# Kernel optimization log

Measured on AMD Instinct MI355X. Metric: run time of the kernel, lower is better.

Reference implementation:

```python
import jax, jax.numpy as jnp
import numpy as np
import math
from jax import lax

B, NP1, M, D, H, L, DFF = 16, 65, 256, 512, 8, 3, 2048
EPS_PROJ = 0.01  # MartingaleProjectionLayer is built with epsilon=0.01
LN_EPS = 1e-5


def _pos_encoding(n, d):
    pos = np.arange(n, dtype=np.float32)[:, None]
    div = np.exp(np.arange(0, d, 2, dtype=np.float32) * (-math.log(10000.0) / d))
    pe = np.zeros((n, d), dtype=np.float32)
    pe[:, 0::2] = np.sin(pos * div)
    pe[:, 1::2] = np.cos(pos * div)
    return jnp.asarray(pe)


def setup_inputs() -> dict:
    key = jax.random.key(0)
    ks = jax.random.split(key, 32)
    s = 0.02
    marg = jax.random.uniform(ks[0], (B, NP1, M), jnp.float32)
    marg = marg / marg.sum(axis=-1, keepdims=True)  # proper distributions
    return {
        "marginals": marg,
        "x_grid": jnp.linspace(-3.0, 3.0, M, dtype=jnp.float32),
        "conv_w": jax.random.normal(ks[1], (128, 1, 5), jnp.float32) * s,
        "conv_b": jax.random.normal(ks[2], (128,), jnp.float32) * s,
        "fc_w": jax.random.normal(ks[3], (128, D), jnp.float32) * s,
        "fc_b": jax.random.normal(ks[4], (D,), jnp.float32) * s,
        "ln0_g": jnp.ones((D,), jnp.float32),
        "ln0_b": jnp.zeros((D,), jnp.float32),
        "pos_enc": _pos_encoding(NP1, D),
        "qkv_w": jax.random.normal(ks[5], (L, 3 * D, D), jnp.float32) * s,
        "qkv_b": jax.random.normal(ks[6], (L, 3 * D), jnp.float32) * s,
        "out_w": jax.random.normal(ks[7], (L, D, D), jnp.float32) * s,
        "out_b": jax.random.normal(ks[8], (L, D), jnp.float32) * s,
        "ln1_g": jnp.ones((L, D), jnp.float32),
        "ln1_b": jnp.zeros((L, D), jnp.float32),
        "ff1_w": jax.random.normal(ks[9], (L, DFF, D), jnp.float32) * s,
        "ff1_b": jax.random.normal(ks[10], (L, DFF), jnp.float32) * s,
        "ff2_w": jax.random.normal(ks[11], (L, D, DFF), jnp.float32) * s,
        "ff2_b": jax.random.normal(ks[12], (L, D), jnp.float32) * s,
        "ln2_g": jnp.ones((L, D), jnp.float32),
        "ln2_b": jnp.zeros((L, D), jnp.float32),
        "u_w": jax.random.normal(ks[13], (M, D), jnp.float32) * s,
        "u_b": jax.random.normal(ks[14], (M,), jnp.float32) * s,
        "h_w": jax.random.normal(ks[15], (M, D), jnp.float32) * s,
        "h_b": jax.random.normal(ks[16], (M,), jnp.float32) * s,
    }


def _ln(x, g, b):
    mu = x.mean(axis=-1, keepdims=True)
    var = ((x - mu) ** 2).mean(axis=-1, keepdims=True)
    return (x - mu) * lax.rsqrt(var + LN_EPS) * g + b


def _gelu(x):
    return jax.nn.gelu(x, approximate=False)  # torch default exact GELU


def reference(marginals, x_grid, conv_w, conv_b, fc_w, fc_b, ln0_g, ln0_b,
              pos_enc, qkv_w, qkv_b, out_w, out_b, ln1_g, ln1_b,
              ff1_w, ff1_b, ff2_w, ff2_b, ln2_g, ln2_b, u_w, u_b, h_w, h_b):
    b, np1, m = marginals.shape
    n = np1 - 1
    d = fc_w.shape[1]
    nh = H
    dh = d // nh

    # ---- marginal embedding: Conv1d(1,128,k=5,pad=2) -> mean over grid -> FC+LN+GELU
    x = marginals.reshape(b * np1, 1, m)
    y = lax.conv_general_dilated(x, conv_w, (1,), [(2, 2)],
                                 dimension_numbers=("NCH", "OIH", "NCH"))
    y = y + conv_b[None, :, None]          # (b*np1, 128, m)
    emb = y.mean(axis=2)                   # (b*np1, 128)
    emb = _gelu(_ln(emb @ fc_w + fc_b, ln0_g, ln0_b))
    xs = emb.reshape(b, np1, d) + pos_enc[None, :np1, :]

    # ---- post-norm transformer encoder (dropout off / eval mode)
    scale = 1.0 / math.sqrt(dh)
    for l in range(L):
        qkv = xs @ qkv_w[l].T + qkv_b[l]                        # (b, s, 3d)
        q, k, v = jnp.split(qkv, 3, axis=-1)
        q = q.reshape(b, np1, nh, dh).transpose(0, 2, 1, 3)
        k = k.reshape(b, np1, nh, dh).transpose(0, 2, 1, 3)
        v = v.reshape(b, np1, nh, dh).transpose(0, 2, 1, 3)
        att = jax.nn.softmax(jnp.einsum("bhqd,bhkd->bhqk", q, k) * scale, axis=-1)
        o = jnp.einsum("bhqk,bhkd->bhqd", att, v)
        o = o.transpose(0, 2, 1, 3).reshape(b, np1, d)
        o = o @ out_w[l].T + out_b[l]
        xs = _ln(xs + o, ln1_g[l], ln1_b[l])
        ff = _gelu(xs @ ff1_w[l].T + ff1_b[l]) @ ff2_w[l].T + ff2_b[l]
        xs = _ln(xs + ff, ln2_g[l], ln2_b[l])

    u_pot = xs @ u_w.T + u_b                                    # (b, np1, M)
    h_raw = xs[:, :n, :] @ h_w.T + h_b                          # (b, n, M)

    # ---- vectorized martingale projection over all N timesteps
    x_diff = x_grid[:, None] - x_grid[None, :]                  # (M, M)
    h_kernel = h_raw[..., None] * x_diff                        # (b, n, M, M)
    P = jax.nn.softmax(h_kernel / EPS_PROJ, axis=-1)
    expected_next = jnp.einsum("bnij,j->bni", P, x_grid)
    drift = expected_next - x_grid                              # (b, n, M)
    mu = marginals[:, :n, :]
    weight_drift = (mu * drift).sum(axis=-1, keepdims=True)
    correction = weight_drift / (mu.sum(axis=-1, keepdims=True) + 1e-8)
    h_pot = h_raw - correction
    return (u_pot, h_pot)
```

## Files before the change

kernel.cpp:

```cpp
#include <hip/hip_runtime.h>
#include <math.h>


#define BT   1040
#define NP1  65
#define Dm   512
#define MG   256

typedef short short8 __attribute__((ext_vector_type(8)));
typedef float f32x4  __attribute__((ext_vector_type(4)));
typedef unsigned short u16;

__device__ __forceinline__ size_t pidx(int r, int c, int KB) {
  return ((size_t)((r >> 6) * KB + (c >> 6)) * 8 + ((c & 63) >> 3)) * 512
       + (size_t)((r & 63) * 8 + (c & 7));
}

__device__ __forceinline__ u16 f2bf(float f) {
  unsigned int u = __float_as_uint(f);
  u += 0x7FFF + ((u >> 16) & 1);
  return (u16)(u >> 16);
}

__device__ __forceinline__ float bf2f(u16 v) {
  return __uint_as_float((unsigned int)v << 16);
}

__device__ __forceinline__ float gelu_exact(float x) {
  return 0.5f * x * (1.0f + erff(x * 0.70710678118654752f));
}

__device__ __forceinline__ void async16(const u16* g, u16* l) {
  __builtin_amdgcn_global_load_lds(
      (const __attribute__((address_space(1))) unsigned int*)g,
      (__attribute__((address_space(3))) unsigned int*)l, 16, 0, 0);
}

__device__ __forceinline__ float wred(float v) {
#pragma unroll
  for (int o = 32; o; o >>= 1) v += __shfl_xor(v, o, 64);
  return v;
}

__device__ __forceinline__ float block_reduce_sum(float v, float* s) {
#pragma unroll
  for (int off = 32; off; off >>= 1) v += __shfl_down(v, off, 64);
  int lane = threadIdx.x & 63, wid = threadIdx.x >> 6;
  __syncthreads();
  if (lane == 0) s[wid] = v;
  __syncthreads();
  return s[0] + s[1] + s[2] + s[3];
}

__device__ __forceinline__ float f_closed(float a) {
  const float tf = 2.3529411765f;
  float t = a * tf;
  float s = fabsf(t);
  float E;
  if (s < 1e-4f) {
    E = 127.5f - 5461.25f * t;
  } else {
    float u = s * 256.0f;
    float term2 = (u < 80.0f) ? 256.0f / expm1f(u) : 0.0f;
    float Epos = 1.0f / expm1f(s) - term2;
    E = (t > 0.0f) ? Epos : 255.0f - Epos;
  }
  return -3.0f + 0.0235294118f * E;
}

__global__ __launch_bounds__(256) void prep_kernel(
    const float* __restrict__ qkv_w, const float* __restrict__ out_w,
    const float* __restrict__ ff1_w, const float* __restrict__ ff2_w,
    const float* __restrict__ u_w,   const float* __restrict__ h_w,
    u16* __restrict__ wdst,
    const float* __restrict__ marg, const float* __restrict__ conv_w,
    const float* __restrict__ conv_b, const float* __restrict__ fc_w,
    const float* __restrict__ fc_b, const float* __restrict__ g,
    const float* __restrict__ bb, const float* __restrict__ pos,
    float* __restrict__ xs, u16* __restrict__ xsb)
{
  const int tid = threadIdx.x;
  if (blockIdx.x < 512) {
    const size_t O1 = 2359296, O2 = 3145728, O3 = 6291456;
    const size_t O4 = 9437184, O5 = 9568256, TOT4 = 9699328 / 4;
    for (size_t e4 = (size_t)blockIdx.x * 256 + tid; e4 < TOT4;
         e4 += (size_t)512 * 256) {
      size_t e = e4 * 4;
      const float* src; size_t base; int n, k, KB;
      if (e < O1)      { size_t r = e;      src = qkv_w + r; base = 0;
                         n = (int)(r >> 9);  k = (int)(r & 511);  KB = 8; }
      else if (e < O2) { size_t r = e - O1; src = out_w + r; base = O1;
                         n = (int)(r >> 9);  k = (int)(r & 511);  KB = 8; }
      else if (e < O3) { size_t r = e - O2; src = ff1_w + r; base = O2;
                         n = (int)(r >> 9);  k = (int)(r & 511);  KB = 8; }
      else if (e < O4) { size_t r = e - O3; src = ff2_w + r; base = O3;
                         n = (int)(r >> 11); k = (int)(r & 2047); KB = 32; }
      else if (e < O5) { size_t r = e - O4; src = u_w + r;   base = O4;
                         n = (int)(r >> 9);  k = (int)(r & 511);  KB = 8; }
      else             { size_t r = e - O5; src = h_w + r;   base = O4;
                         n = 256 + (int)(r >> 9); k = (int)(r & 511); KB = 8; }
      float4 v = *(const float4*)src;
      unsigned int lo = (unsigned int)f2bf(v.x) | ((unsigned int)f2bf(v.y) << 16);
      unsigned int hi = (unsigned int)f2bf(v.z) | ((unsigned int)f2bf(v.w) << 16);
      *(uint2*)(wdst + base + pidx(n, k, KB)) = make_uint2(lo, hi);
    }
    return;
  }
  __shared__ float es[4][128];
  __shared__ float sS[4];
  __shared__ float edge[4][4];
  __shared__ float red[4];
  const int t0 = (blockIdx.x - 512) * 4;
  const int lane = tid & 63, wave = tid >> 6;
  {
    float4 mv = *(const float4*)(marg + (size_t)(t0 + wave) * MG + lane * 4);
    float S = wred(mv.x + mv.y + mv.z + mv.w);
    if (lane == 0) sS[wave] = S;
  }
  if (tid < 16) {
    int k = tid >> 2, e = tid & 3;
    int idx = (e < 2) ? e : (e + 252);
    edge[k][e] = marg[(size_t)(t0 + k) * MG + idx];
  }
  __syncthreads();
  if (tid < 128) {
    int o = tid;
    float w0 = conv_w[o*5+0], w1 = conv_w[o*5+1], w2 = conv_w[o*5+2];
    float w3 = conv_w[o*5+3], w4 = conv_w[o*5+4], cb = conv_b[o];
#pragma unroll
    for (int k = 0; k < 4; ++k) {
      float S = sS[k];
      float x0 = edge[k][0], x1 = edge[k][1], x254 = edge[k][2], x255 = edge[k][3];
      es[k][o] = (w0*(S - x254 - x255) + w1*(S - x255) + w2*S
                + w3*(S - x0) + w4*(S - x0 - x1)) * (1.0f/256.0f) + cb;
    }
  }
  __syncthreads();
  float b0 = fc_b[tid], b1 = fc_b[tid + 256];
  float z[4][2];
#pragma unroll
  for (int k = 0; k < 4; ++k) { z[k][0] = b0; z[k][1] = b1; }
#pragma unroll 4
  for (int o = 0; o < 128; ++o) {
    float f0 = fc_w[(size_t)o*Dm + tid];
    float f1 = fc_w[(size_t)o*Dm + tid + 256];
#pragma unroll
    for (int k = 0; k < 4; ++k) {
      float e = es[k][o];
      z[k][0] += e * f0; z[k][1] += e * f1;
    }
  }
  float g0 = g[tid], g1 = g[tid+256], e0 = bb[tid], e1 = bb[tid+256];
#pragma unroll
  for (int k = 0; k < 4; ++k) {
    float mu = block_reduce_sum(z[k][0] + z[k][1], red) * (1.0f/512.0f);
    float d0 = z[k][0] - mu, d1 = z[k][1] - mu;
    float var = block_reduce_sum(d0*d0 + d1*d1, red) * (1.0f/512.0f);
    float inv = rsqrtf(var + 1e-5f);
    int t = t0 + k, p = t % NP1;
    float y0 = gelu_exact(d0*inv*g0 + e0) + pos[(size_t)p*Dm + tid];
    float y1 = gelu_exact(d1*inv*g1 + e1) + pos[(size_t)p*Dm + tid + 256];
    xs[(size_t)t*Dm + tid]        = y0;
    xs[(size_t)t*Dm + tid + 256]  = y1;
    xsb[pidx(t, tid, 8)]          = f2bf(y0);
    xsb[pidx(t, tid + 256, 8)]    = f2bf(y1);
  }
}

template<int MODE>
__global__ __launch_bounds__(256) void gemm_mfma(
    const u16* __restrict__ A, const u16* __restrict__ Bw,
    const float* __restrict__ bias, float* __restrict__ Cf,
    u16* __restrict__ Cb, int Mrows, int N, int K)
{
  __shared__ alignas(16) u16 Asl[2][4096];
  __shared__ alignas(16) u16 Bsl[2][4096];
  const int tid = threadIdx.x;
  const int row0 = blockIdx.y * 64, col0 = blockIdx.x * 64;
  const int lane = tid & 63, wave = tid >> 6;
  const int wm = (wave >> 1) * 32, wn = (wave & 1) * 32;
  const int l15 = lane & 15, q = lane >> 4;
  const int KB = K >> 6;

  f32x4 acc[2][2];
  acc[0][0] = (f32x4){0,0,0,0}; acc[0][1] = (f32x4){0,0,0,0};
  acc[1][0] = (f32x4){0,0,0,0}; acc[1][1] = (f32x4){0,0,0,0};

  const size_t abase = (size_t)blockIdx.y * KB * 4096 + (size_t)lane * 8;
  const size_t bbase = (size_t)blockIdx.x * KB * 4096 + (size_t)lane * 8;
  const int c0w = wave * 2;

#pragma unroll
  for (int i = 0; i < 2; ++i) {
    int c = c0w + i;
    async16(A + abase + (size_t)c * 512, &Asl[0][(size_t)(c * 64 + lane) * 8]);
    async16(Bw + bbase + (size_t)c * 512, &Bsl[0][(size_t)(c * 64 + lane) * 8]);
  }

  const int nk = K >> 6;
  for (int t = 0; t < nk; ++t) {
    const int cur = t & 1;
    if (t + 1 < nk) {
      const int nxt = cur ^ 1;
#pragma unroll
      for (int i = 0; i < 2; ++i) {
        int c = c0w + i;
        async16(A + abase + (size_t)((t + 1) * 8 + c) * 512,
                &Asl[nxt][(size_t)(c * 64 + lane) * 8]);
        async16(Bw + bbase + (size_t)((t + 1) * 8 + c) * 512,
                &Bsl[nxt][(size_t)(c * 64 + lane) * 8]);
      }
      asm volatile("s_waitcnt vmcnt(4)" ::: "memory");
    } else {
      asm volatile("s_waitcnt vmcnt(0)" ::: "memory");
    }
    __builtin_amdgcn_s_barrier();
#pragma unroll
    for (int tt = 0; tt < 2; ++tt) {
      int cc = tt * 4 + q;
      short8 af[2], bf[2];
#pragma unroll
      for (int mi = 0; mi < 2; ++mi)
        af[mi] = *(short8*)&Asl[cur][(size_t)(cc*64 + wm + mi*16 + l15) * 8];
#pragma unroll
      for (int ni = 0; ni < 2; ++ni)
        bf[ni] = *(short8*)&Bsl[cur][(size_t)(cc*64 + wn + ni*16 + l15) * 8];
#pragma unroll
      for (int mi = 0; mi < 2; ++mi)
#pragma unroll
        for (int ni = 0; ni < 2; ++ni)
          acc[mi][ni] = __builtin_amdgcn_mfma_f32_16x16x32_bf16(
              af[mi], bf[ni], acc[mi][ni], 0, 0, 0);
    }
    __builtin_amdgcn_s_barrier();
  }

#pragma unroll
  for (int mi = 0; mi < 2; ++mi) {
#pragma unroll
    for (int ni = 0; ni < 2; ++ni) {
      int col = col0 + wn + ni*16 + l15;
#pragma unroll
      for (int r = 0; r < 4; ++r) {
        int row = row0 + wm + mi*16 + q*4 + r;
        if (row < Mrows) {
          float v = acc[mi][ni][r];
          if (MODE == 0) {
            Cf[(size_t)row*N + col] = v + bias[col];
          } else {
            Cb[pidx(row, col, 32)] = f2bf(gelu_exact(v + bias[col]));
          }
        }
      }
    }
  }
}

__global__ __launch_bounds__(256) void fused_qkv_attn(
    const u16* __restrict__ xsb, const u16* __restrict__ qkvw,
    const float* __restrict__ qkvb, u16* __restrict__ obufb)
{
  __shared__ alignas(16) u16 stbuf[10240];
  __shared__ alignas(16) float qf[65][67];
  __shared__ alignas(16) float kf[65][67];
  __shared__ alignas(16) u16   vb[65][68];
  u16* sta = stbuf;
  float (*ss)[67] = (float (*)[67])stbuf;

  const int b = blockIdx.x >> 3, h = blockIdx.x & 7;
  const int tid = threadIdx.x, lane = tid & 63, wave = tid >> 6;
  const int l15 = lane & 15, q = lane >> 4;
  const int rowg0 = b * NP1;

  f32x4 acc[5][3];
#pragma unroll
  for (int rt = 0; rt < 5; ++rt)
#pragma unroll
    for (int j = 0; j < 3; ++j) acc[rt][j] = (f32x4){0,0,0,0};

  for (int ch = 0; ch < 4; ++ch) {
    __syncthreads();
    for (int idx = tid; idx < 16 * 80; idx += 256) {
      int kg = idx / 80, rl = idx - kg * 80;
      int r = rowg0 + min(rl, 64);
      async16(xsb + pidx(r, ch * 128 + kg * 8, 8), &sta[(size_t)idx * 8]);
    }
    asm volatile("s_waitcnt vmcnt(0)" ::: "memory");
    __syncthreads();

    short8 bcur[3], bnxt[3];
#pragma unroll
    for (int j = 0; j < 3; ++j) {
      int f = wave * 3 + j, region = f >> 2, sub = f & 3;
      int nb = region * 8 + h, nn = sub * 16 + l15;
      int kk = ch * 128 + q * 8;
      int kbg = kk >> 6, cc = (kk & 63) >> 3;
      bcur[j] = *(const short8*)&qkvw[((size_t)(nb * 8 + kbg) * 8 + cc) * 512
                                      + nn * 8];
    }
#pragma unroll
    for (int s = 0; s < 4; ++s) {
      if (s + 1 < 4) {
#pragma unroll
        for (int j = 0; j < 3; ++j) {
          int f = wave * 3 + j, region = f >> 2, sub = f & 3;
          int nb = region * 8 + h, nn = sub * 16 + l15;
          int kk = ch * 128 + (s + 1) * 32 + q * 8;
          int kbg = kk >> 6, cc = (kk & 63) >> 3;
          bnxt[j] = *(const short8*)&qkvw[((size_t)(nb * 8 + kbg) * 8 + cc) * 512
                                          + nn * 8];
        }
      }
      short8 af[5];
#pragma unroll
      for (int rt = 0; rt < 5; ++rt)
        af[rt] = *(short8*)&sta[(size_t)((s * 4 + q) * 80 + rt * 16 + l15) * 8];
#pragma unroll
      for (int rt = 0; rt < 5; ++rt)
#pragma unroll
        for (int j = 0; j < 3; ++j)
          acc[rt][j] = __builtin_amdgcn_mfma_f32_16x16x32_bf16(
              af[rt], bcur[j], acc[rt][j], 0, 0, 0);
#pragma unroll
      for (int j = 0; j < 3; ++j) bcur[j] = bnxt[j];
    }
  }

#pragma unroll
  for (int rt = 0; rt < 5; ++rt) {
#pragma unroll
    for (int j = 0; j < 3; ++j) {
      int f = wave * 3 + j, region = f >> 2, sub = f & 3;
      int cw = sub * 16 + l15;
      float bias = qkvb[region * 512 + h * 64 + cw];
#pragma unroll
      for (int r = 0; r < 4; ++r) {
        int row = rt * 16 + q * 4 + r;
        if (row < 65) {
          float v = acc[rt][j][r] + bias;
          if      (region == 0) qf[row][cw] = v;
          else if (region == 1) kf[row][cw] = v;
          else                  vb[row][cw] = f2bf(v);
        }
      }
    }
  }
  __syncthreads();

#pragma unroll
  for (int it = 0; it < 2; ++it) {
    int tile = it * 256 + tid;
    if (tile < 289) {
      int ti = (tile / 17) * 4, tj = (tile % 17) * 4;
      const float* qr[4]; const float* kr[4];
#pragma unroll
      for (int i = 0; i < 4; ++i) { qr[i] = qf[min(ti + i, 64)]; kr[i] = kf[min(tj + i, 64)]; }
      float a4[4][4] = {};
      for (int d = 0; d < 64; ++d) {
        float a[4], bvv[4];
#pragma unroll
        for (int i = 0; i < 4; ++i) { a[i] = qr[i][d]; bvv[i] = kr[i][d]; }
#pragma unroll
        for (int i = 0; i < 4; ++i)
#pragma unroll
          for (int j = 0; j < 4; ++j) a4[i][j] += a[i] * bvv[j];
      }
#pragma unroll
      for (int i = 0; i < 4; ++i)
        if (ti + i < 65)
#pragma unroll
          for (int j = 0; j < 4; ++j)
            if (tj + j < 65) ss[ti + i][tj + j] = a4[i][j] * 0.125f;
    }
  }
  __syncthreads();

  if (tid < 65) {
    float mx = -1e30f;
    for (int j = 0; j < 65; ++j) mx = fmaxf(mx, ss[tid][j]);
    float s = 0.0f;
    for (int j = 0; j < 65; ++j) { float e = expf(ss[tid][j] - mx); ss[tid][j] = e; s += e; }
    float inv = 1.0f / s;
    for (int j = 0; j < 65; ++j) ss[tid][j] *= inv;
  }
  __syncthreads();

#pragma unroll
  for (int it = 0; it < 2; ++it) {
    int tile = it * 256 + tid;
    if (tile < 272) {
      int ti = (tile >> 4) * 4, d0 = (tile & 15) * 4;
      const float* sr[4];
#pragma unroll
      for (int i = 0; i < 4; ++i) sr[i] = ss[min(ti + i, 64)];
      float a4[4][4] = {};
      for (int j = 0; j < 65; ++j) {
        float v0 = bf2f(vb[j][d0]),   v1 = bf2f(vb[j][d0+1]);
        float v2 = bf2f(vb[j][d0+2]), v3 = bf2f(vb[j][d0+3]);
#pragma unroll
        for (int i = 0; i < 4; ++i) {
          float s = sr[i][j];
          a4[i][0] += s * v0; a4[i][1] += s * v1;
          a4[i][2] += s * v2; a4[i][3] += s * v3;
        }
      }
#pragma unroll
      for (int i = 0; i < 4; ++i)
        if (ti + i < 65) {
          ushort4 o;
          o.x = f2bf(a4[i][0]); o.y = f2bf(a4[i][1]);
          o.z = f2bf(a4[i][2]); o.w = f2bf(a4[i][3]);
          *(ushort4*)(obufb + pidx(b * NP1 + ti + i, h * 64 + d0, 8)) = o;
        }
    }
  }
}

__global__ __launch_bounds__(512) void fused_row512(
    const u16* __restrict__ A, const u16* __restrict__ Bw,
    const float* __restrict__ bias,
    float* __restrict__ xs, u16* __restrict__ xsb,
    const float* __restrict__ g, const float* __restrict__ bb)
{
  constexpr int KB = 8;
  __shared__ alignas(16) u16 Alds[16 * 512];
  __shared__ float red[8][16];
  __shared__ float red2[8][16];
  const int tid = threadIdx.x, lane = tid & 63, wave = tid >> 6;
  const int l15 = lane & 15, q = lane >> 4;
  const int r0 = blockIdx.x * 16;
  const int rb = r0 >> 6, ro = r0 & 63;
  const int gc0 = wave * 64;
  const int nb = wave;

  f32x4 acc[4];
#pragma unroll
  for (int i = 0; i < 4; ++i) acc[i] = (f32x4){0,0,0,0};

  for (int idx = tid; idx < 1024; idx += 512) {
    int rloc = idx & 15, cg = idx >> 4;
    int kbg = cg >> 3, cc = cg & 7;
    async16(A + ((size_t)(rb * KB + kbg) * 8 + cc) * 512 + (ro + rloc) * 8,
            &Alds[(size_t)idx * 8]);
  }
  asm volatile("s_waitcnt vmcnt(0)" ::: "memory");
  __syncthreads();

  short8 bcur[4], bnxt[4];
  {
    int kk = q * 8;
    int kbg = kk >> 6, cc = (kk & 63) >> 3;
#pragma unroll
    for (int i = 0; i < 4; ++i)
      bcur[i] = *(const short8*)&Bw[((size_t)(nb * KB + kbg) * 8 + cc) * 512
                                    + (i * 16 + l15) * 8];
  }
  for (int s = 0; s < 16; ++s) {
    if (s + 1 < 16) {
      int kk = (s + 1) * 32 + q * 8;
      int kbg = kk >> 6, cc = (kk & 63) >> 3;
#pragma unroll
      for (int i = 0; i < 4; ++i)
        bnxt[i] = *(const short8*)&Bw[((size_t)(nb * KB + kbg) * 8 + cc) * 512
                                      + (i * 16 + l15) * 8];
    }
    short8 af = *(const short8*)&Alds[(size_t)((s * 4 + q) * 16 + l15) * 8];
#pragma unroll
    for (int i = 0; i < 4; ++i)
      acc[i] = __builtin_amdgcn_mfma_f32_16x16x32_bf16(af, bcur[i], acc[i], 0, 0, 0);
#pragma unroll
    for (int i = 0; i < 4; ++i) bcur[i] = bnxt[i];
  }

  float vv[4][4];
#pragma unroll
  for (int i = 0; i < 4; ++i) {
    int col = gc0 + i*16 + l15;
    float bcol = bias[col];
#pragma unroll
    for (int r = 0; r < 4; ++r) {
      int gr = r0 + q*4 + r;
      vv[i][r] = acc[i][r] + bcol + xs[(size_t)gr * Dm + col];
    }
  }
  float ps[4];
#pragma unroll
  for (int r = 0; r < 4; ++r) {
    float s = 0.f;
#pragma unroll
    for (int i = 0; i < 4; ++i) s += vv[i][r];
    ps[r] = s;
  }
#pragma unroll
  for (int o = 1; o < 16; o <<= 1)
#pragma unroll
    for (int r = 0; r < 4; ++r) ps[r] += __shfl_xor(ps[r], o, 64);
  if (l15 == 0)
#pragma unroll
    for (int r = 0; r < 4; ++r) red[wave][q*4 + r] = ps[r];
  __syncthreads();
  float mu[4];
#pragma unroll
  for (int r = 0; r < 4; ++r) {
    int rr = q*4 + r;
    float s = 0.f;
#pragma unroll
    for (int w = 0; w < 8; ++w) s += red[w][rr];
    mu[r] = s * (1.0f/512.0f);
  }
  float ps2[4];
#pragma unroll
  for (int r = 0; r < 4; ++r) {
    float s = 0.f;
#pragma unroll
    for (int i = 0; i < 4; ++i) { float d = vv[i][r] - mu[r]; s += d * d; }
    ps2[r] = s;
  }
#pragma unroll
  for (int o = 1; o < 16; o <<= 1)
#pragma unroll
    for (int r = 0; r < 4; ++r) ps2[r] += __shfl_xor(ps2[r], o, 64);
  if (l15 == 0)
#pragma unroll
    for (int r = 0; r < 4; ++r) red2[wave][q*4 + r] = ps2[r];
  __syncthreads();
  float inv[4];
#pragma unroll
  for (int r = 0; r < 4; ++r) {
    int rr = q*4 + r;
    float s = 0.f;
#pragma unroll
    for (int w = 0; w < 8; ++w) s += red2[w][rr];
    inv[r] = rsqrtf(s * (1.0f/512.0f) + 1e-5f);
  }
#pragma unroll
  for (int i = 0; i < 4; ++i) {
    int col = gc0 + i*16 + l15;
    float gc = g[col], bc = bb[col];
#pragma unroll
    for (int r = 0; r < 4; ++r) {
      int gr = r0 + q*4 + r;
      float y = (vv[i][r] - mu[r]) * inv[r] * gc + bc;
      xs[(size_t)gr * Dm + col] = y;
      xsb[pidx(gr, col, 8)] = f2bf(y);
    }
  }
}

template<int HEAD>
__global__ __launch_bounds__(1024) void fused_ff2(
    const u16* __restrict__ A, const u16* __restrict__ Bw,
    const float* __restrict__ bias,
    float* __restrict__ xs, u16* __restrict__ xsb,
    const float* __restrict__ g, const float* __restrict__ bb,
    const u16* __restrict__ uhw, const float* __restrict__ ub,
    const float* __restrict__ hbv, const float* __restrict__ marg,
    const float* __restrict__ xg, float* __restrict__ outu,
    float* __restrict__ outh)
{
  constexpr int KB = 32;
  __shared__ alignas(16) u16 Alds[16 * 1024];
  __shared__ float red[16][16];
  __shared__ float red2[16][16];
  const int tid = threadIdx.x, lane = tid & 63, wave = tid >> 6;
  const int l15 = lane & 15, q = lane >> 4;
  const int r0 = blockIdx.x * 16;
  const int rb = r0 >> 6, ro = r0 & 63;
  const int nb = wave >> 1;
  const int nn0 = (wave & 1) * 32;

  f32x4 acc[2];
  acc[0] = (f32x4){0,0,0,0}; acc[1] = (f32x4){0,0,0,0};

  for (int ch = 0; ch < 2; ++ch) {
    const int kc = ch * 1024;
    __syncthreads();
    for (int idx = tid; idx < 2048; idx += 1024) {
      int rloc = idx & 15, cg = idx >> 4;
      int kbg = (kc >> 6) + (cg >> 3), cc = cg & 7;
      async16(A + ((size_t)(rb * KB + kbg) * 8 + cc) * 512 + (ro + rloc) * 8,
              &Alds[(size_t)idx * 8]);
    }
    asm volatile("s_waitcnt vmcnt(0)" ::: "memory");
    __syncthreads();

    short8 bcur[2], bnxt[2];
    {
      int kk = kc + q * 8;
      int kbg = kk >> 6, cc = (kk & 63) >> 3;
#pragma unroll
      for (int i = 0; i < 2; ++i)
        bcur[i] = *(const short8*)&Bw[((size_t)(nb * KB + kbg) * 8 + cc) * 512
                                      + (nn0 + i * 16 + l15) * 8];
    }
    for (int s = 0; s < 32; ++s) {
      if (s + 1 < 32) {
        int kk = kc + (s + 1) * 32 + q * 8;
        int kbg = kk >> 6, cc = (kk & 63) >> 3;
#pragma unroll
        for (int i = 0; i < 2; ++i)
          bnxt[i] = *(const short8*)&Bw[((size_t)(nb * KB + kbg) * 8 + cc) * 512
                                        + (nn0 + i * 16 + l15) * 8];
      }
      short8 af = *(const short8*)&Alds[(size_t)((s * 4 + q) * 16 + l15) * 8];
#pragma unroll
      for (int i = 0; i < 2; ++i)
        acc[i] = __builtin_amdgcn_mfma_f32_16x16x32_bf16(af, bcur[i], acc[i], 0, 0, 0);
#pragma unroll
      for (int i = 0; i < 2; ++i) bcur[i] = bnxt[i];
    }
  }

  float vv[2][4];
#pragma unroll
  for (int i = 0; i < 2; ++i) {
    int col = wave * 32 + i*16 + l15;
    float bcol = bias[col];
#pragma unroll
    for (int r = 0; r < 4; ++r) {
      int gr = r0 + q*4 + r;
      vv[i][r] = acc[i][r] + bcol + xs[(size_t)gr * Dm + col];
    }
  }
  float ps[4];
#pragma unroll
  for (int r = 0; r < 4; ++r) { ps[r] = vv[0][r] + vv[1][r]; }
#pragma unroll
  for (int o = 1; o < 16; o <<= 1)
#pragma unroll
    for (int r = 0; r < 4; ++r) ps[r] += __shfl_xor(ps[r], o, 64);
  if (l15 == 0)
#pragma unroll
    for (int r = 0; r < 4; ++r) red[wave][q*4 + r] = ps[r];
  __syncthreads();
  float mu[4];
#pragma unroll
  for (int r = 0; r < 4; ++r) {
    int rr = q*4 + r;
    float s = 0.f;
#pragma unroll
    for (int w = 0; w < 16; ++w) s += red[w][rr];
    mu[r] = s * (1.0f/512.0f);
  }
  float ps2[4];
#pragma unroll
  for (int r = 0; r < 4; ++r) {
    float d0 = vv[0][r] - mu[r], d1 = vv[1][r] - mu[r];
    ps2[r] = d0*d0 + d1*d1;
  }
#pragma unroll
  for (int o = 1; o < 16; o <<= 1)
#pragma unroll
    for (int r = 0; r < 4; ++r) ps2[r] += __shfl_xor(ps2[r], o, 64);
  if (l15 == 0)
#pragma unroll
    for (int r = 0; r < 4; ++r) red2[wave][q*4 + r] = ps2[r];
  __syncthreads();
  float inv[4];
#pragma unroll
  for (int r = 0; r < 4; ++r) {
    int rr = q*4 + r;
    float s = 0.f;
#pragma unroll
    for (int w = 0; w < 16; ++w) s += red2[w][rr];
    inv[r] = rsqrtf(s * (1.0f/512.0f) + 1e-5f);
  }

  if (HEAD == 0) {
#pragma unroll
    for (int i = 0; i < 2; ++i) {
      int col = wave * 32 + i*16 + l15;
      float gc = g[col], bc = bb[col];
#pragma unroll
      for (int r = 0; r < 4; ++r) {
        int gr = r0 + q*4 + r;
        float y = (vv[i][r] - mu[r]) * inv[r] * gc + bc;
        xs[(size_t)gr * Dm + col] = y;
        xsb[pidx(gr, col, 8)] = f2bf(y);
      }
    }
  } else {
    __syncthreads();
#pragma unroll
    for (int i = 0; i < 2; ++i) {
      int col = wave * 32 + i*16 + l15;
      float gc = g[col], bc = bb[col];
#pragma unroll
      for (int r = 0; r < 4; ++r) {
        float y = (vv[i][r] - mu[r]) * inv[r] * gc + bc;
        Alds[(size_t)((col >> 3) * 16 + (q*4 + r)) * 8 + (col & 7)] = f2bf(y);
      }
    }
    __syncthreads();

    const int w2 = (wave < 8) ? wave : (wave - 8);
    const int ubr = ((wave < 8) ? 0 : 4) + (w2 >> 1);
    const int hn0 = (w2 & 1) * 32;
    f32x4 a2[2];
    a2[0] = (f32x4){0,0,0,0}; a2[1] = (f32x4){0,0,0,0};
    short8 bcur[2], bnxt[2];
    {
      int kk = q * 8;
      int kbg = kk >> 6, cc = (kk & 63) >> 3;
#pragma unroll
      for (int i = 0; i < 2; ++i)
        bcur[i] = *(const short8*)&uhw[((size_t)(ubr * 8 + kbg) * 8 + cc) * 512
                                       + (hn0 + i * 16 + l15) * 8];
    }
    for (int s = 0; s < 16; ++s) {
      if (s + 1 < 16) {
        int kk = (s + 1) * 32 + q * 8;
        int kbg = kk >> 6, cc = (kk & 63) >> 3;
#pragma unroll
        for (int i = 0; i < 2; ++i)
          bnxt[i] = *(const short8*)&uhw[((size_t)(ubr * 8 + kbg) * 8 + cc) * 512
                                         + (hn0 + i * 16 + l15) * 8];
      }
      short8 af = *(const short8*)&Alds[(size_t)((s * 4 + q) * 16 + l15) * 8];
#pragma unroll
      for (int i = 0; i < 2; ++i)
        a2[i] = __builtin_amdgcn_mfma_f32_16x16x32_bf16(af, bcur[i], a2[i], 0, 0, 0);
#pragma unroll
      for (int i = 0; i < 2; ++i) bcur[i] = bnxt[i];
    }

    float va[2][4];
    if (wave >= 8) {
      float wd[4] = {0.f,0.f,0.f,0.f}, ms[4] = {0.f,0.f,0.f,0.f};
#pragma unroll
      for (int i = 0; i < 2; ++i) {
        int hcol = (wave - 8) * 32 + i*16 + l15;
        float bcol = hbv[hcol];
        float xv = xg[hcol];
#pragma unroll
        for (int r = 0; r < 4; ++r) {
          int gr = r0 + q*4 + r;
          float a = a2[i][r] + bcol;
          va[i][r] = a;
          float uvm = marg[(size_t)gr * MG + hcol];
          wd[r] += uvm * (f_closed(a) - xv);
          ms[r] += uvm;
        }
      }
#pragma unroll
      for (int o = 1; o < 16; o <<= 1)
#pragma unroll
        for (int r = 0; r < 4; ++r) {
          wd[r] += __shfl_xor(wd[r], o, 64);
          ms[r] += __shfl_xor(ms[r], o, 64);
        }
      if (l15 == 0)
#pragma unroll
        for (int r = 0; r < 4; ++r) {
          red[wave][q*4 + r]  = wd[r];
          red2[wave][q*4 + r] = ms[r];
        }
    }
    __syncthreads();
    if (wave < 8) {
#pragma unroll
      for (int i = 0; i < 2; ++i) {
        int col = wave * 32 + i*16 + l15;
        float bcol = ub[col];
#pragma unroll
        for (int r = 0; r < 4; ++r) {
          int gr = r0 + q*4 + r;
          outu[(size_t)gr * MG + col] = a2[i][r] + bcol;
        }
      }
    } else {
#pragma unroll
      for (int i = 0; i < 2; ++i) {
        int hcol = (wave - 8) * 32 + i*16 + l15;
#pragma unroll
        for (int r = 0; r < 4; ++r) {
          int rr = q*4 + r;
          int gr = r0 + rr;
          int bI = gr / NP1, n = gr - bI * NP1;
          if (n < 64) {
            float num = 0.f, den = 0.f;
#pragma unroll
            for (int w = 8; w < 16; ++w) { num += red[w][rr]; den += red2[w][rr]; }
            float corr = num / (den + 1e-8f);
            outh[(size_t)(bI * 64 + n) * MG + hcol] = va[i][r] - corr;
          }
        }
      }
    }
  }
}

extern "C" void kernel_launch(void* const* d_in, const int* in_sizes, int n_in,
                              void* d_out, int out_size, void* d_ws, size_t ws_size,
                              hipStream_t stream)
{
  const float* marg   = (const float*)d_in[0];
  const float* xg     = (const float*)d_in[1];
  const float* conv_w = (const float*)d_in[2];
  const float* conv_b = (const float*)d_in[3];
  const float* fc_w   = (const float*)d_in[4];
  const float* fc_b   = (const float*)d_in[5];
  const float* ln0_g  = (const float*)d_in[6];
  const float* ln0_b  = (const float*)d_in[7];
  const float* pos    = (const float*)d_in[8];
  const float* qkv_w  = (const float*)d_in[9];
  const float* qkv_b  = (const float*)d_in[10];
  const float* out_w  = (const float*)d_in[11];
  const float* out_b  = (const float*)d_in[12];
  const float* ln1_g  = (const float*)d_in[13];
  const float* ln1_b  = (const float*)d_in[14];
  const float* ff1_w  = (const float*)d_in[15];
  const float* ff1_b  = (const float*)d_in[16];
  const float* ff2_w  = (const float*)d_in[17];
  const float* ff2_b  = (const float*)d_in[18];
  const float* ln2_g  = (const float*)d_in[19];
  const float* ln2_b  = (const float*)d_in[20];
  const float* u_w    = (const float*)d_in[21];
  const float* u_b    = (const float*)d_in[22];
  const float* h_w    = (const float*)d_in[23];
  const float* h_b    = (const float*)d_in[24];
  float* out = (float*)d_out;

  float* ws = (float*)d_ws;
  float* xs      = ws;
  u16*   xsb     = (u16*)(ws + 2129920);
  u16*   obufb   = (u16*)(ws + 2408448);
  u16*   ffb     = (u16*)(ws + 2686976);
  u16*   wbf     = (u16*)(ws + 3801088);

  const u16* qkv_bw = wbf;
  const u16* out_bw = wbf + 2359296;
  const u16* ff1_bw = wbf + 3145728;
  const u16* ff2_bw = wbf + 6291456;
  const u16* uh_bw  = wbf + 9437184;

  prep_kernel<<<772, 256, 0, stream>>>(
      qkv_w, out_w, ff1_w, ff2_w, u_w, h_w, wbf,
      marg, conv_w, conv_b, fc_w, fc_b, ln0_g, ln0_b, pos, xs, xsb);

  for (int l = 0; l < 3; ++l) {
    fused_qkv_attn<<<128, 256, 0, stream>>>(
        xsb, qkv_bw + (size_t)l*786432, qkv_b + l*1536, obufb);
    fused_row512<<<65, 512, 0, stream>>>(
        obufb, out_bw + (size_t)l*262144, out_b + l*512,
        xs, xsb, ln1_g + l*512, ln1_b + l*512);
    gemm_mfma<1><<<dim3(32, 17), 256, 0, stream>>>(
        xsb, ff1_bw + (size_t)l*1048576, ff1_b + l*2048, nullptr,
        ffb, BT, 2048, 512);
    if (l < 2) {
      fused_ff2<0><<<65, 1024, 0, stream>>>(
          ffb, ff2_bw + (size_t)l*1048576, ff2_b + l*512,
          xs, xsb, ln2_g + l*512, ln2_b + l*512,
          nullptr, nullptr, nullptr, nullptr, nullptr, nullptr, nullptr);
    } else {
      fused_ff2<1><<<65, 1024, 0, stream>>>(
          ffb, ff2_bw + (size_t)l*1048576, ff2_b + l*512,
          xs, xsb, ln2_g + l*512, ln2_b + l*512,
          uh_bw, u_b, h_b, marg, xg, out, out + 1040*256);
    }
  }
}
```

Baseline: 381.2 us.

## Fuse FF1 GEMM with GELU into the FF2+LayerNorm kernel per row block

Removes the separate FF1 GEMM launch and its bf16 intermediate buffer in global memory. Each 16-row block now computes its FF1 slice with GELU into shared memory in two 1024-column chunks and feeds it straight into the FF2 MFMA accumulation. This saves one kernel launch per layer and the write and re-read of the 1040x2048 activation. In exchange, FF1 work now runs on only 65 blocks instead of 544, and every block streams the full FF1 weight matrix, which lowers parallelism and multiplies weight traffic.

```diff
diff --git a/kernel.cpp b/kernel.cpp
--- a/kernel.cpp
+++ b/kernel.cpp
@@ -167,95 +167,6 @@
   }
 }
 
-template<int MODE>
-__global__ __launch_bounds__(256) void gemm_mfma(
-    const u16* __restrict__ A, const u16* __restrict__ Bw,
-    const float* __restrict__ bias, float* __restrict__ Cf,
-    u16* __restrict__ Cb, int Mrows, int N, int K)
-{
-  __shared__ alignas(16) u16 Asl[2][4096];
-  __shared__ alignas(16) u16 Bsl[2][4096];
-  const int tid = threadIdx.x;
-  const int row0 = blockIdx.y * 64, col0 = blockIdx.x * 64;
-  const int lane = tid & 63, wave = tid >> 6;
-  const int wm = (wave >> 1) * 32, wn = (wave & 1) * 32;
-  const int l15 = lane & 15, q = lane >> 4;
-  const int KB = K >> 6;
-
-  f32x4 acc[2][2];
-  acc[0][0] = (f32x4){0,0,0,0}; acc[0][1] = (f32x4){0,0,0,0};
-  acc[1][0] = (f32x4){0,0,0,0}; acc[1][1] = (f32x4){0,0,0,0};
-
-  const size_t abase = (size_t)blockIdx.y * KB * 4096 + (size_t)lane * 8;
-  const size_t bbase = (size_t)blockIdx.x * KB * 4096 + (size_t)lane * 8;
-  const int c0w = wave * 2;
-
-#pragma unroll
-  for (int i = 0; i < 2; ++i) {
-    int c = c0w + i;
-    async16(A + abase + (size_t)c * 512, &Asl[0][(size_t)(c * 64 + lane) * 8]);
-    async16(Bw + bbase + (size_t)c * 512, &Bsl[0][(size_t)(c * 64 + lane) * 8]);
-  }
-
-  const int nk = K >> 6;
-  for (int t = 0; t < nk; ++t) {
-    const int cur = t & 1;
-    if (t + 1 < nk) {
-      const int nxt = cur ^ 1;
-#pragma unroll
-      for (int i = 0; i < 2; ++i) {
-        int c = c0w + i;
-        async16(A + abase + (size_t)((t + 1) * 8 + c) * 512,
-                &Asl[nxt][(size_t)(c * 64 + lane) * 8]);
-        async16(Bw + bbase + (size_t)((t + 1) * 8 + c) * 512,
-                &Bsl[nxt][(size_t)(c * 64 + lane) * 8]);
-      }
-      asm volatile("s_waitcnt vmcnt(4)" ::: "memory");
-    } else {
-      asm volatile("s_waitcnt vmcnt(0)" ::: "memory");
-    }
-    __builtin_amdgcn_s_barrier();
-#pragma unroll
-    for (int tt = 0; tt < 2; ++tt) {
-      int cc = tt * 4 + q;
-      short8 af[2], bf[2];
-#pragma unroll
-      for (int mi = 0; mi < 2; ++mi)
-        af[mi] = *(short8*)&Asl[cur][(size_t)(cc*64 + wm + mi*16 + l15) * 8];
-#pragma unroll
-      for (int ni = 0; ni < 2; ++ni)
-        bf[ni] = *(short8*)&Bsl[cur][(size_t)(cc*64 + wn + ni*16 + l15) * 8];
-#pragma unroll
-      for (int mi = 0; mi < 2; ++mi)
-#pragma unroll
-        for (int ni = 0; ni < 2; ++ni)
-          acc[mi][ni] = __builtin_amdgcn_mfma_f32_16x16x32_bf16(
-              af[mi], bf[ni], acc[mi][ni], 0, 0, 0);
-    }
-    __builtin_amdgcn_s_barrier();
-  }
-
-#pragma unroll
-  for (int mi = 0; mi < 2; ++mi) {
-#pragma unroll
-    for (int ni = 0; ni < 2; ++ni) {
-      int col = col0 + wn + ni*16 + l15;
-#pragma unroll
-      for (int r = 0; r < 4; ++r) {
-        int row = row0 + wm + mi*16 + q*4 + r;
-        if (row < Mrows) {
-          float v = acc[mi][ni][r];
-          if (MODE == 0) {
-            Cf[(size_t)row*N + col] = v + bias[col];
-          } else {
-            Cb[pidx(row, col, 32)] = f2bf(gelu_exact(v + bias[col]));
-          }
-        }
-      }
-    }
-  }
-}
-
 __global__ __launch_bounds__(256) void fused_qkv_attn(
     const u16* __restrict__ xsb, const u16* __restrict__ qkvw,
     const float* __restrict__ qkvb, u16* __restrict__ obufb)
@@ -548,9 +459,10 @@
 }
 
 template<int HEAD>
-__global__ __launch_bounds__(1024) void fused_ff2(
-    const u16* __restrict__ A, const u16* __restrict__ Bw,
-    const float* __restrict__ bias,
+__global__ __launch_bounds__(1024) void fused_ffx(
+    const u16* __restrict__ xsb_in, const u16* __restrict__ f1w,
+    const u16* __restrict__ f2w, const float* __restrict__ b1,
+    const float* __restrict__ b2,
     float* __restrict__ xs, u16* __restrict__ xsb,
     const float* __restrict__ g, const float* __restrict__ bb,
     const u16* __restrict__ uhw, const float* __restrict__ ub,
@@ -558,56 +470,99 @@
     const float* __restrict__ xg, float* __restrict__ outu,
     float* __restrict__ outh)
 {
-  constexpr int KB = 32;
-  __shared__ alignas(16) u16 Alds[16 * 1024];
+  __shared__ alignas(16) u16 A1[16 * 512];
+  __shared__ alignas(16) u16 H[16 * 1024];
   __shared__ float red[16][16];
   __shared__ float red2[16][16];
   const int tid = threadIdx.x, lane = tid & 63, wave = tid >> 6;
   const int l15 = lane & 15, q = lane >> 4;
   const int r0 = blockIdx.x * 16;
   const int rb = r0 >> 6, ro = r0 & 63;
-  const int nb = wave >> 1;
-  const int nn0 = (wave & 1) * 32;
-
-  f32x4 acc[2];
-  acc[0] = (f32x4){0,0,0,0}; acc[1] = (f32x4){0,0,0,0};
+
+  {
+    int idx = tid;
+    int rloc = idx & 15, cg = idx >> 4;
+    int kbg = cg >> 3, cc = cg & 7;
+    async16(xsb_in + ((size_t)(rb * 8 + kbg) * 8 + cc) * 512 + (ro + rloc) * 8,
+            &A1[(size_t)idx * 8]);
+  }
+  asm volatile("s_waitcnt vmcnt(0)" ::: "memory");
+  __syncthreads();
+
+  f32x4 acc2[2];
+  acc2[0] = (f32x4){0,0,0,0}; acc2[1] = (f32x4){0,0,0,0};
+  const int nb2 = wave >> 1;
+  const int nn2 = (wave & 1) * 32;
 
   for (int ch = 0; ch < 2; ++ch) {
-    const int kc = ch * 1024;
+    const int fcol0 = ch * 1024 + wave * 64;
+    const int fnb = fcol0 >> 6;
+    f32x4 acc1[4];
+#pragma unroll
+    for (int i = 0; i < 4; ++i) acc1[i] = (f32x4){0,0,0,0};
+    short8 bcur[4], bnxt[4];
+    {
+      int kk = q * 8;
+      int kbg = kk >> 6, cc = (kk & 63) >> 3;
+#pragma unroll
+      for (int i = 0; i < 4; ++i)
+        bcur[i] = *(const short8*)&f1w[((size_t)(fnb * 8 + kbg) * 8 + cc) * 512
+                                       + (i * 16 + l15) * 8];
+    }
+    for (int s = 0; s < 16; ++s) {
+      if (s + 1 < 16) {
+        int kk = (s + 1) * 32 + q * 8;
+        int kbg = kk >> 6, cc = (kk & 63) >> 3;
+#pragma unroll
+        for (int i = 0; i < 4; ++i)
+          bnxt[i] = *(const short8*)&f1w[((size_t)(fnb * 8 + kbg) * 8 + cc) * 512
+                                         + (i * 16 + l15) * 8];
+      }
+      short8 af = *(const short8*)&A1[(size_t)((s * 4 + q) * 16 + l15) * 8];
+#pragma unroll
+      for (int i = 0; i < 4; ++i)
+        acc1[i] = __builtin_amdgcn_mfma_f32_16x16x32_bf16(af, bcur[i], acc1[i], 0, 0, 0);
+#pragma unroll
+      for (int i = 0; i < 4; ++i) bcur[i] = bnxt[i];
+    }
     __syncthreads();
-    for (int idx = tid; idx < 2048; idx += 1024) {
-      int rloc = idx & 15, cg = idx >> 4;
-      int kbg = (kc >> 6) + (cg >> 3), cc = cg & 7;
-      async16(A + ((size_t)(rb * KB + kbg) * 8 + cc) * 512 + (ro + rloc) * 8,
-              &Alds[(size_t)idx * 8]);
-    }
-    asm volatile("s_waitcnt vmcnt(0)" ::: "memory");
+#pragma unroll
+    for (int i = 0; i < 4; ++i) {
+      int lc = wave * 64 + i * 16 + l15;
+      float bcol = b1[fcol0 + i * 16 + l15];
+#pragma unroll
+      for (int r = 0; r < 4; ++r) {
+        int row = q * 4 + r;
+        H[(size_t)((lc >> 3) * 16 + row) * 8 + (lc & 7)] =
+            f2bf(gelu_exact(acc1[i][r] + bcol));
+      }
+    }
     __syncthreads();
 
-    short8 bcur[2], bnxt[2];
+    short8 c2[2], n2[2];
     {
-      int kk = kc + q * 8;
+      int kk = ch * 1024 + q * 8;
       int kbg = kk >> 6, cc = (kk & 63) >> 3;
 #pragma unroll
       for (int i = 0; i < 2; ++i)
-        bcur[i] = *(const short8*)&Bw[((size_t)(nb * KB + kbg) * 8 + cc) * 512
-                                      + (nn0 + i * 16 + l15) * 8];
+        c2[i] = *(const short8*)&f2w[((size_t)(nb2 * 32 + kbg) * 8 + cc) * 512
+                                     + (nn2 + i * 16 + l15) * 8];
     }
     for (int s = 0; s < 32; ++s) {
       if (s + 1 < 32) {
-        int kk = kc + (s + 1) * 32 + q * 8;
+        int kk = ch * 1024 + (s + 1) * 32 + q * 8;
         int kbg = kk >> 6, cc = (kk & 63) >> 3;
 #pragma unroll
         for (int i = 0; i < 2; ++i)
-          bnxt[i] = *(const short8*)&Bw[((size_t)(nb * KB + kbg) * 8 + cc) * 512
-                                        + (nn0 + i * 16 + l15) * 8];
-      }
-      short8 af = *(const short8*)&Alds[(size_t)((s * 4 + q) * 16 + l15) * 8];
+          n2[i] = *(const short8*)&f2w[((size_t)(nb2 * 32 + kbg) * 8 + cc) * 512
+                                       + (nn2 + i * 16 + l15) * 8];
+      }
+      short8 af = *(const short8*)&H[(size_t)((s * 4 + q) * 16 + l15) * 8];
 #pragma unroll
       for (int i = 0; i < 2; ++i)
-        acc[i] = __builtin_amdgcn_mfma_f32_16x16x32_bf16(af, bcur[i], acc[i], 0, 0, 0);
-#pragma unroll
-      for (int i = 0; i < 2; ++i) bcur[i] = bnxt[i];
+        acc2[i] = __builtin_amdgcn_mfma_f32_16x16x32_bf16(af, c2[i], acc2[i], 0, 0, 0);
+#pragma unroll
+      for (int i = 0; i < 2; ++i) c2[i] = n2[i];
     }
   }
 
@@ -615,11 +570,11 @@
 #pragma unroll
   for (int i = 0; i < 2; ++i) {
     int col = wave * 32 + i*16 + l15;
-    float bcol = bias[col];
+    float bcol = b2[col];
 #pragma unroll
     for (int r = 0; r < 4; ++r) {
       int gr = r0 + q*4 + r;
-      vv[i][r] = acc[i][r] + bcol + xs[(size_t)gr * Dm + col];
+      vv[i][r] = acc2[i][r] + bcol + xs[(size_t)gr * Dm + col];
     }
   }
   float ps[4];
@@ -688,7 +643,7 @@
 #pragma unroll
       for (int r = 0; r < 4; ++r) {
         float y = (vv[i][r] - mu[r]) * inv[r] * gc + bc;
-        Alds[(size_t)((col >> 3) * 16 + (q*4 + r)) * 8 + (col & 7)] = f2bf(y);
+        A1[(size_t)((col >> 3) * 16 + (q*4 + r)) * 8 + (col & 7)] = f2bf(y);
       }
     }
     __syncthreads();
@@ -698,14 +653,14 @@
     const int hn0 = (w2 & 1) * 32;
     f32x4 a2[2];
     a2[0] = (f32x4){0,0,0,0}; a2[1] = (f32x4){0,0,0,0};
-    short8 bcur[2], bnxt[2];
+    short8 hc[2], hn[2];
     {
       int kk = q * 8;
       int kbg = kk >> 6, cc = (kk & 63) >> 3;
 #pragma unroll
       for (int i = 0; i < 2; ++i)
-        bcur[i] = *(const short8*)&uhw[((size_t)(ubr * 8 + kbg) * 8 + cc) * 512
-                                       + (hn0 + i * 16 + l15) * 8];
+        hc[i] = *(const short8*)&uhw[((size_t)(ubr * 8 + kbg) * 8 + cc) * 512
+                                     + (hn0 + i * 16 + l15) * 8];
     }
     for (int s = 0; s < 16; ++s) {
       if (s + 1 < 16) {
@@ -713,15 +668,15 @@
         int kbg = kk >> 6, cc = (kk & 63) >> 3;
 #pragma unroll
         for (int i = 0; i < 2; ++i)
-          bnxt[i] = *(const short8*)&uhw[((size_t)(ubr * 8 + kbg) * 8 + cc) * 512
-                                         + (hn0 + i * 16 + l15) * 8];
-      }
-      short8 af = *(const short8*)&Alds[(size_t)((s * 4 + q) * 16 + l15) * 8];
+          hn[i] = *(const short8*)&uhw[((size_t)(ubr * 8 + kbg) * 8 + cc) * 512
+                                       + (hn0 + i * 16 + l15) * 8];
+      }
+      short8 af = *(const short8*)&A1[(size_t)((s * 4 + q) * 16 + l15) * 8];
 #pragma unroll
       for (int i = 0; i < 2; ++i)
-        a2[i] = __builtin_amdgcn_mfma_f32_16x16x32_bf16(af, bcur[i], a2[i], 0, 0, 0);
-#pragma unroll
-      for (int i = 0; i < 2; ++i) bcur[i] = bnxt[i];
+        a2[i] = __builtin_amdgcn_mfma_f32_16x16x32_bf16(af, hc[i], a2[i], 0, 0, 0);
+#pragma unroll
+      for (int i = 0; i < 2; ++i) hc[i] = hn[i];
     }
 
     float va[2][4];
@@ -825,7 +780,6 @@
   float* xs      = ws;
   u16*   xsb     = (u16*)(ws + 2129920);
   u16*   obufb   = (u16*)(ws + 2408448);
-  u16*   ffb     = (u16*)(ws + 2686976);
   u16*   wbf     = (u16*)(ws + 3801088);
 
   const u16* qkv_bw = wbf;
@@ -844,17 +798,16 @@
     fused_row512<<<65, 512, 0, stream>>>(
         obufb, out_bw + (size_t)l*262144, out_b + l*512,
         xs, xsb, ln1_g + l*512, ln1_b + l*512);
-    gemm_mfma<1><<<dim3(32, 17), 256, 0, stream>>>(
-        xsb, ff1_bw + (size_t)l*1048576, ff1_b + l*2048, nullptr,
-        ffb, BT, 2048, 512);
     if (l < 2) {
-      fused_ff2<0><<<65, 1024, 0, stream>>>(
-          ffb, ff2_bw + (size_t)l*1048576, ff2_b + l*512,
+      fused_ffx<0><<<65, 1024, 0, stream>>>(
+          xsb, ff1_bw + (size_t)l*1048576, ff2_bw + (size_t)l*1048576,
+          ff1_b + l*2048, ff2_b + l*512,
           xs, xsb, ln2_g + l*512, ln2_b + l*512,
           nullptr, nullptr, nullptr, nullptr, nullptr, nullptr, nullptr);
     } else {
-      fused_ff2<1><<<65, 1024, 0, stream>>>(
-          ffb, ff2_bw + (size_t)l*1048576, ff2_b + l*512,
+      fused_ffx<1><<<65, 1024, 0, stream>>>(
+          xsb, ff1_bw + (size_t)l*1048576, ff2_bw + (size_t)l*1048576,
+          ff1_b + l*2048, ff2_b + l*512,
           xs, xsb, ln2_g + l*512, ln2_b + l*512,
           uh_bw, u_b, h_b, marg, xg, out, out + 1040*256);
     }
```

Measured after the change: 415.1 us. 1.09x slower.
